# Performance work log

Hardware: AMD Instinct MI355X
Metric: run time of the kernel (lower is better)

Reference implementation:

```python
import jax, jax.numpy as jnp
import numpy as np

DIM = 4096
N_HEADS = 32
N_KV_HEADS = 8
HEAD_DIM = DIM // N_HEADS  # 128
N_REP = N_HEADS // N_KV_HEADS  # 4
MAX_BS = 16
MAX_SEQ = 4096
SEQLEN = 1
START_POS = 4095
ROPE_THETA = 500000.0


def setup_inputs() -> dict:
    key = jax.random.key(0)
    ks = jax.random.split(key, 8)
    w_scale = 0.02  # keep logits in a sane range
    x = jax.random.normal(ks[0], (MAX_BS, SEQLEN, DIM), dtype=jnp.float32)
    wq = jax.random.normal(ks[1], (DIM, N_HEADS * HEAD_DIM), dtype=jnp.float32) * w_scale
    wk = jax.random.normal(ks[2], (DIM, N_KV_HEADS * HEAD_DIM), dtype=jnp.float32) * w_scale
    wv = jax.random.normal(ks[3], (DIM, N_KV_HEADS * HEAD_DIM), dtype=jnp.float32) * w_scale
    wo = jax.random.normal(ks[4], (N_HEADS * HEAD_DIM, DIM), dtype=jnp.float32) * w_scale
    cache_k = jax.random.normal(ks[5], (MAX_BS, MAX_SEQ, N_KV_HEADS, HEAD_DIM), dtype=jnp.float32)
    cache_v = jax.random.normal(ks[6], (MAX_BS, MAX_SEQ, N_KV_HEADS, HEAD_DIM), dtype=jnp.float32)
    # true rotary frequencies for positions [START_POS, START_POS+SEQLEN)
    inv_freq = 1.0 / (ROPE_THETA ** (np.arange(0, HEAD_DIM, 2, dtype=np.float32) / HEAD_DIM))  # [hd/2]
    t = np.arange(START_POS, START_POS + SEQLEN, dtype=np.float32)[:, None]  # [s,1]
    angles = t * inv_freq[None, :]  # [s, hd/2]
    freqs_cos = jnp.asarray(np.cos(angles), dtype=jnp.float32)
    freqs_sin = jnp.asarray(np.sin(angles), dtype=jnp.float32)
    return {"x": x, "wq": wq, "wk": wk, "wv": wv, "wo": wo,
            "cache_k": cache_k, "cache_v": cache_v,
            "freqs_cos": freqs_cos, "freqs_sin": freqs_sin,
            "start_pos": START_POS}


def _rope(t, cos, sin):
    # t: [b, s, h, hd]; cos/sin: [s, hd/2] -> broadcast [1, s, 1, hd/2]
    b, s, h, hd = t.shape
    tp = t.reshape(b, s, h, hd // 2, 2)
    e, o = tp[..., 0], tp[..., 1]
    c = cos[None, :, None, :]
    sn = sin[None, :, None, :]
    re = e * c - o * sn
    im = e * sn + o * c
    return jnp.stack([re, im], axis=-1).reshape(b, s, h, hd)


def reference(x, wq, wk, wv, wo, cache_k, cache_v, freqs_cos, freqs_sin, start_pos):
    bsz, seqlen, _ = x.shape
    xq = (x @ wq).reshape(bsz, seqlen, N_HEADS, HEAD_DIM)
    xk = (x @ wk).reshape(bsz, seqlen, N_KV_HEADS, HEAD_DIM)
    xv = (x @ wv).reshape(bsz, seqlen, N_KV_HEADS, HEAD_DIM)
    xq = _rope(xq, freqs_cos, freqs_sin)
    xk = _rope(xk, freqs_cos, freqs_sin)
    # KV-cache append
    cache_k = jax.lax.dynamic_update_slice(cache_k, xk, (0, start_pos, 0, 0))
    cache_v = jax.lax.dynamic_update_slice(cache_v, xv, (0, start_pos, 0, 0))
    kv_len = start_pos + seqlen  # static Python int
    keys = cache_k[:, :kv_len]    # [b, t, g, hd]
    values = cache_v[:, :kv_len]  # [b, t, g, hd]
    # GQA via broadcasting (math-equivalent to repeat_kv)
    q = xq.reshape(bsz, seqlen, N_KV_HEADS, N_REP, HEAD_DIM)
    scale = 1.0 / jnp.sqrt(jnp.float32(HEAD_DIM))
    scores = jnp.einsum('bsgrh,btgh->bgrst', q, keys) * scale  # [b,g,r,s,t]
    probs = jax.nn.softmax(scores.astype(jnp.float32), axis=-1).astype(xq.dtype)
    out = jnp.einsum('bgrst,btgh->bsgrh', probs, values)  # [b,s,g,r,hd]
    out = out.reshape(bsz, seqlen, N_HEADS * HEAD_DIM)
    return out @ wo
```

## Files before the change

### kernel.cpp

```cpp
#include <hip/hip_runtime.h>
#include <math.h>

#define DIM    4096
#define NH     32
#define NKV    8
#define HD     128
#define BS     16
#define KVLEN  4096
#define LASTPOS 4095
#define QKV_COLS 6144
#define NKC    64

typedef float f32x4 __attribute__((ext_vector_type(4)));

#define WS_QKV   0
#define WS_ATTN  98304
#define WS_PART  163840
#define WS_PQ    2326528
#define WS_PW    8617984

__global__ __launch_bounds__(256) void qkv_projA(
    const float* __restrict__ x, const float* __restrict__ wq,
    const float* __restrict__ wk, const float* __restrict__ wv,
    float* __restrict__ pq) {
  __shared__ float xs[16 * 64];
  const int tid = threadIdx.x;
  const int col = (blockIdx.x * 256 + tid) * 2;
  const int kc = blockIdx.y;
  const int k0 = kc * 64;

  for (int i = tid; i < 1024; i += 256) {
    int b = i >> 6, k = i & 63;
    xs[i] = x[b * DIM + k0 + k];
  }
  __syncthreads();

  const float* w;
  int wstride, wcol;
  if (col < 4096)      { w = wq; wstride = 4096; wcol = col; }
  else if (col < 5120) { w = wk; wstride = 1024; wcol = col - 4096; }
  else                 { w = wv; wstride = 1024; wcol = col - 5120; }
  const float* wp = w + (size_t)k0 * wstride + wcol;

  float acc0[16], acc1[16];
#pragma unroll
  for (int b = 0; b < 16; ++b) { acc0[b] = 0.f; acc1[b] = 0.f; }

#pragma unroll 2
  for (int k = 0; k < 64; k += 4) {
    float2 w0 = *(const float2*)(wp + (size_t)(k + 0) * wstride);
    float2 w1 = *(const float2*)(wp + (size_t)(k + 1) * wstride);
    float2 w2 = *(const float2*)(wp + (size_t)(k + 2) * wstride);
    float2 w3 = *(const float2*)(wp + (size_t)(k + 3) * wstride);
#pragma unroll
    for (int b = 0; b < 16; ++b) {
      float4 xb = *(const float4*)(&xs[b * 64 + k]);
      acc0[b] += xb.x * w0.x + xb.y * w1.x + xb.z * w2.x + xb.w * w3.x;
      acc1[b] += xb.x * w0.y + xb.y * w1.y + xb.z * w2.y + xb.w * w3.y;
    }
  }
#pragma unroll
  for (int b = 0; b < 16; ++b) {
    *(float2*)(&pq[((size_t)kc * 16 + b) * QKV_COLS + col]) = make_float2(acc0[b], acc1[b]);
  }
}

__global__ __launch_bounds__(256) void qkv_projB(
    const float* __restrict__ pq, float* __restrict__ qkv,
    const float* __restrict__ fc, const float* __restrict__ fs) {
  int t = blockIdx.x * 256 + threadIdx.x;
  int b = t / 3072, pr = t % 3072;
  int col = 2 * pr;
  float e = 0.f, o = 0.f;
#pragma unroll 8
  for (int kc = 0; kc < NKC; ++kc) {
    float2 v = *(const float2*)(&pq[((size_t)kc * 16 + b) * QKV_COLS + col]);
    e += v.x; o += v.y;
  }
  float re = e, im = o;
  if (col < 5120) {
    int i = (col & 127) >> 1;
    float c = fc[i], s = fs[i];
    float scale = (col < 4096) ? 0.08838834764831845f : 1.0f;
    re = (e * c - o * s) * scale;
    im = (e * s + o * c) * scale;
  }
  *(float2*)(&qkv[b * QKV_COLS + col]) = make_float2(re, im);
}

__global__ __launch_bounds__(256, 4) void attn_partial(
    const float* __restrict__ cache_k, const float* __restrict__ cache_v,
    const float* __restrict__ qkv, float* __restrict__ part) {
  __shared__ float red[4][4][130];
  const int tid = threadIdx.x;
  const int w = tid >> 6, lane = tid & 63;
  const int p = lane >> 4, ql = lane & 15;
  const int chunk = blockIdx.x & 31;
  const int bg = blockIdx.x >> 5;
  const int b = bg >> 3, g = bg & 7;
  const int t0w = chunk * 128 + w * 32;

  const float* qbase = qkv + b * QKV_COLS + g * 512;
  f32x4 qA[4], qB[4];
#pragma unroll
  for (int h = 0; h < 4; ++h) {
    qA[h] = *(const f32x4*)(qbase + h * 128 + ql * 4);
    qB[h] = *(const f32x4*)(qbase + h * 128 + 64 + ql * 4);
  }

  const float* kbase = cache_k + ((size_t)b * 4096 * 8 + g) * 128;
  const float* xk    = qkv + b * QKV_COLS + 4096 + g * 128;

  float sv8[8];
#pragma unroll
  for (int it = 0; it < 8; ++it) {
    int t = t0w + it * 4 + p;
    const float* krow = (t == LASTPOS) ? xk : (kbase + (size_t)t * 1024);
    f32x4 k0 = *(const f32x4*)(krow + ql * 4);
    f32x4 k1 = *(const f32x4*)(krow + 64 + ql * 4);
    float s[4];
#pragma unroll
    for (int h = 0; h < 4; ++h) {
      s[h] = k0[0]*qA[h][0] + k0[1]*qA[h][1] + k0[2]*qA[h][2] + k0[3]*qA[h][3]
           + k1[0]*qB[h][0] + k1[1]*qB[h][1] + k1[2]*qB[h][2] + k1[3]*qB[h][3];
    }
#pragma unroll
    for (int off = 1; off < 16; off <<= 1) {
#pragma unroll
      for (int h = 0; h < 4; ++h) s[h] += __shfl_xor(s[h], off);
    }
    int hsel = ql & 3;
    float v = s[0];
    if (hsel == 1) v = s[1];
    if (hsel == 2) v = s[2];
    if (hsel == 3) v = s[3];
    sv8[it] = v;
  }

  float m = -1e30f;
#pragma unroll
  for (int it = 0; it < 8; ++it) m = fmaxf(m, sv8[it]);
  m = fmaxf(m, __shfl_xor(m, 16));
  m = fmaxf(m, __shfl_xor(m, 32));
  float l = 0.f;
#pragma unroll
  for (int it = 0; it < 8; ++it) { sv8[it] = __expf(sv8[it] - m); l += sv8[it]; }
  l += __shfl_xor(l, 16);
  l += __shfl_xor(l, 32);

  const float* vbase = cache_v + ((size_t)b * 4096 * 8 + g) * 128;
  const float* xv    = qkv + b * QKV_COLS + 5120 + g * 128;
  const int h2 = lane >> 5;
  const int dq = lane & 31;
  f32x4 acc[4];
#pragma unroll
  for (int h = 0; h < 4; ++h) acc[h] = (f32x4)(0.f);

#pragma unroll
  for (int jj = 0; jj < 16; ++jj) {
    int lr = 2 * jj + h2;
    int t = t0w + lr;
    const float* vrow = (t == LASTPOS) ? xv : (vbase + (size_t)t * 1024);
    f32x4 vv = *(const f32x4*)(vrow + dq * 4);
    float sreg = sv8[jj >> 1];
    int srcb = (lr & 3) << 4;
    float p0 = __shfl(sreg, srcb + 0);
    float p1 = __shfl(sreg, srcb + 1);
    float p2 = __shfl(sreg, srcb + 2);
    float p3 = __shfl(sreg, srcb + 3);
    acc[0] += p0 * vv;
    acc[1] += p1 * vv;
    acc[2] += p2 * vv;
    acc[3] += p3 * vv;
  }
#pragma unroll
  for (int h = 0; h < 4; ++h) {
    acc[h][0] += __shfl_xor(acc[h][0], 32);
    acc[h][1] += __shfl_xor(acc[h][1], 32);
    acc[h][2] += __shfl_xor(acc[h][2], 32);
    acc[h][3] += __shfl_xor(acc[h][3], 32);
  }
  if (lane < 32) {
#pragma unroll
    for (int h = 0; h < 4; ++h)
      *(f32x4*)(&red[w][h][dq * 4]) = acc[h];
  }
  if (lane < 4) { red[w][lane][128] = m; red[w][lane][129] = l; }
  __syncthreads();

  for (int item = tid; item < 512; item += 256) {
    int h = item >> 7, d = item & 127;
    float M = -1e30f;
#pragma unroll
    for (int w2 = 0; w2 < 4; ++w2) M = fmaxf(M, red[w2][h][128]);
    float num = 0.f, den = 0.f;
#pragma unroll
    for (int w2 = 0; w2 < 4; ++w2) {
      float wgt = __expf(red[w2][h][128] - M);
      num += wgt * red[w2][h][d];
      den += wgt * red[w2][h][129];
    }
    size_t pi = ((size_t)blockIdx.x * 4 + h) * 132;
    part[pi + d] = num;
    if (d == 0) { part[pi + 128] = M; part[pi + 129] = den; }
  }
}

__global__ __launch_bounds__(256) void attn_combine(
    const float* __restrict__ part, float* __restrict__ attn_out) {
  int t = blockIdx.x * 256 + threadIdx.x;
  int d = t & 127, h = (t >> 7) & 3, bg = t >> 9;
  int b = bg >> 3, g = bg & 7;
  float M = -1e30f;
  float ms[32];
#pragma unroll
  for (int c = 0; c < 32; ++c) {
    ms[c] = part[((size_t)(bg * 32 + c) * 4 + h) * 132 + 128];
    M = fmaxf(M, ms[c]);
  }
  float num = 0.f, den = 0.f;
#pragma unroll 4
  for (int c = 0; c < 32; ++c) {
    const float* pr = part + ((size_t)(bg * 32 + c) * 4 + h) * 132;
    float wgt = __expf(ms[c] - M);
    num += wgt * pr[d];
    den += wgt * pr[129];
  }
  attn_out[b * DIM + (g * 4 + h) * 128 + d] = num / den;
}

__global__ __launch_bounds__(256) void out_projA(
    const float* __restrict__ attn, const float* __restrict__ wo,
    float* __restrict__ pw) {
  __shared__ float xs[16 * 64];
  const int tid = threadIdx.x;
  const int col = (blockIdx.x * 256 + tid) * 2;
  const int kc = blockIdx.y;
  const int k0 = kc * 64;

  for (int i = tid; i < 1024; i += 256) {
    int b = i >> 6, k = i & 63;
    xs[i] = attn[b * DIM + k0 + k];
  }
  __syncthreads();

  const float* wp = wo + (size_t)k0 * 4096 + col;
  float acc0[16], acc1[16];
#pragma unroll
  for (int b = 0; b < 16; ++b) { acc0[b] = 0.f; acc1[b] = 0.f; }

#pragma unroll 2
  for (int k = 0; k < 64; k += 4) {
    float2 w0 = *(const float2*)(wp + (size_t)(k + 0) * 4096);
    float2 w1 = *(const float2*)(wp + (size_t)(k + 1) * 4096);
    float2 w2 = *(const float2*)(wp + (size_t)(k + 2) * 4096);
    float2 w3 = *(const float2*)(wp + (size_t)(k + 3) * 4096);
#pragma unroll
    for (int b = 0; b < 16; ++b) {
      float4 xb = *(const float4*)(&xs[b * 64 + k]);
      acc0[b] += xb.x * w0.x + xb.y * w1.x + xb.z * w2.x + xb.w * w3.x;
      acc1[b] += xb.x * w0.y + xb.y * w1.y + xb.z * w2.y + xb.w * w3.y;
    }
  }
#pragma unroll
  for (int b = 0; b < 16; ++b) {
    *(float2*)(&pw[((size_t)kc * 16 + b) * DIM + col]) = make_float2(acc0[b], acc1[b]);
  }
}

__global__ __launch_bounds__(256) void out_projB(
    const float* __restrict__ pw, float* __restrict__ out) {
  int t = blockIdx.x * 256 + threadIdx.x;
  int b = t >> 12, col = t & 4095;
  float sum = 0.f;
#pragma unroll 8
  for (int kc = 0; kc < NKC; ++kc)
    sum += pw[((size_t)kc * 16 + b) * DIM + col];
  out[b * DIM + col] = sum;
}

extern "C" void kernel_launch(void* const* d_in, const int* in_sizes, int n_in,
                              void* d_out, int out_size, void* d_ws, size_t ws_size,
                              hipStream_t stream) {
  const float* x  = (const float*)d_in[0];
  const float* wq = (const float*)d_in[1];
  const float* wk = (const float*)d_in[2];
  const float* wv = (const float*)d_in[3];
  const float* wo = (const float*)d_in[4];
  const float* ck = (const float*)d_in[5];
  const float* cv = (const float*)d_in[6];
  const float* fc = (const float*)d_in[7];
  const float* fs = (const float*)d_in[8];

  float* ws_f  = (float*)d_ws;
  float* qkv   = ws_f + WS_QKV;
  float* attn  = ws_f + WS_ATTN;
  float* part  = ws_f + WS_PART;
  float* pq    = ws_f + WS_PQ;
  float* pw    = ws_f + WS_PW;
  float* out   = (float*)d_out;

  qkv_projA<<<dim3(12, NKC), 256, 0, stream>>>(x, wq, wk, wv, pq);
  qkv_projB<<<192, 256, 0, stream>>>(pq, qkv, fc, fs);
  attn_partial<<<4096, 256, 0, stream>>>(ck, cv, qkv, part);
  attn_combine<<<256, 256, 0, stream>>>(part, attn);
  out_projA<<<dim3(8, NKC), 256, 0, stream>>>(attn, wo, pw);
  out_projB<<<256, 256, 0, stream>>>(pw, out);
}
```

Measured before the change: 195.2 us.

## Stage KV rows in LDS with register prefetch and online softmax across chunks

The attention partial kernel now has each 512-thread block cover one batch and all 8 KV groups over a 64-token chunk. Contiguous 4 KB KV rows are loaded with fully coalesced vector loads into shared memory, and the next 8-row stage is prefetched into registers while the current one is computed. Softmax is done online across stages, and the in-block cross-wave reduction is dropped; each wave writes its own partial. The combine kernel now merges 64 chunk partials per group with a streaming rescale. This trades the previous strided per-group global loads for better coalescing, at the cost of more partials, extra barriers and heavy LDS use (64 KB) that limits occupancy.

```diff
diff --git a/kernel.cpp b/kernel.cpp
--- a/kernel.cpp
+++ b/kernel.cpp
@@ -10,14 +10,17 @@
 #define LASTPOS 4095
 #define QKV_COLS 6144
 #define NKC    64
+#define TCHUNK 64
+#define NCHK   64
+#define NSTG   8
 
 typedef float f32x4 __attribute__((ext_vector_type(4)));
 
 #define WS_QKV   0
 #define WS_ATTN  98304
 #define WS_PART  163840
-#define WS_PQ    2326528
-#define WS_PW    8617984
+#define WS_PQ    4489216
+#define WS_PW    10780672
 
 __global__ __launch_bounds__(256) void qkv_projA(
     const float* __restrict__ x, const float* __restrict__ wq,
@@ -88,19 +91,20 @@
   *(float2*)(&qkv[b * QKV_COLS + col]) = make_float2(re, im);
 }
 
-__global__ __launch_bounds__(256, 4) void attn_partial(
+__global__ __launch_bounds__(512, 4) void attn_partial(
     const float* __restrict__ cache_k, const float* __restrict__ cache_v,
     const float* __restrict__ qkv, float* __restrict__ part) {
-  __shared__ float red[4][4][130];
+  __shared__ float ks[8192];
+  __shared__ float vs[8192];
   const int tid = threadIdx.x;
   const int w = tid >> 6, lane = tid & 63;
   const int p = lane >> 4, ql = lane & 15;
-  const int chunk = blockIdx.x & 31;
-  const int bg = blockIdx.x >> 5;
-  const int b = bg >> 3, g = bg & 7;
-  const int t0w = chunk * 128 + w * 32;
-
-  const float* qbase = qkv + b * QKV_COLS + g * 512;
+  const int hsel = ql & 3;
+  const int chunk = blockIdx.x & (NCHK - 1);
+  const int b = blockIdx.x >> 6;
+  const int t0 = chunk * TCHUNK;
+
+  const float* qbase = qkv + b * QKV_COLS + w * 512;
   f32x4 qA[4], qB[4];
 #pragma unroll
   for (int h = 0; h < 4; ++h) {
@@ -108,71 +112,115 @@
     qB[h] = *(const f32x4*)(qbase + h * 128 + 64 + ql * 4);
   }
 
-  const float* kbase = cache_k + ((size_t)b * 4096 * 8 + g) * 128;
-  const float* xk    = qkv + b * QKV_COLS + 4096 + g * 128;
-
-  float sv8[8];
-#pragma unroll
-  for (int it = 0; it < 8; ++it) {
-    int t = t0w + it * 4 + p;
-    const float* krow = (t == LASTPOS) ? xk : (kbase + (size_t)t * 1024);
-    f32x4 k0 = *(const f32x4*)(krow + ql * 4);
-    f32x4 k1 = *(const f32x4*)(krow + 64 + ql * 4);
-    float s[4];
-#pragma unroll
-    for (int h = 0; h < 4; ++h) {
-      s[h] = k0[0]*qA[h][0] + k0[1]*qA[h][1] + k0[2]*qA[h][2] + k0[3]*qA[h][3]
-           + k1[0]*qB[h][0] + k1[1]*qB[h][1] + k1[2]*qB[h][2] + k1[3]*qB[h][3];
-    }
-#pragma unroll
-    for (int off = 1; off < 16; off <<= 1) {
-#pragma unroll
-      for (int h = 0; h < 4; ++h) s[h] += __shfl_xor(s[h], off);
-    }
-    int hsel = ql & 3;
-    float v = s[0];
-    if (hsel == 1) v = s[1];
-    if (hsel == 2) v = s[2];
-    if (hsel == 3) v = s[3];
-    sv8[it] = v;
-  }
-
-  float m = -1e30f;
-#pragma unroll
-  for (int it = 0; it < 8; ++it) m = fmaxf(m, sv8[it]);
-  m = fmaxf(m, __shfl_xor(m, 16));
-  m = fmaxf(m, __shfl_xor(m, 32));
-  float l = 0.f;
-#pragma unroll
-  for (int it = 0; it < 8; ++it) { sv8[it] = __expf(sv8[it] - m); l += sv8[it]; }
-  l += __shfl_xor(l, 16);
-  l += __shfl_xor(l, 32);
-
-  const float* vbase = cache_v + ((size_t)b * 4096 * 8 + g) * 128;
-  const float* xv    = qkv + b * QKV_COLS + 5120 + g * 128;
-  const int h2 = lane >> 5;
-  const int dq = lane & 31;
+  const float* kroot = cache_k + (size_t)b * 4096 * 1024;
+  const float* vroot = cache_v + (size_t)b * 4096 * 1024;
+  const float* xk = qkv + b * QKV_COLS + 4096;
+  const float* xv = qkv + b * QKV_COLS + 5120;
+
+  float m = -1e30f, l = 0.f;
   f32x4 acc[4];
 #pragma unroll
   for (int h = 0; h < 4; ++h) acc[h] = (f32x4)(0.f);
 
-#pragma unroll
-  for (int jj = 0; jj < 16; ++jj) {
-    int lr = 2 * jj + h2;
-    int t = t0w + lr;
-    const float* vrow = (t == LASTPOS) ? xv : (vbase + (size_t)t * 1024);
-    f32x4 vv = *(const f32x4*)(vrow + dq * 4);
-    float sreg = sv8[jj >> 1];
-    int srcb = (lr & 3) << 4;
-    float p0 = __shfl(sreg, srcb + 0);
-    float p1 = __shfl(sreg, srcb + 1);
-    float p2 = __shfl(sreg, srcb + 2);
-    float p3 = __shfl(sreg, srcb + 3);
-    acc[0] += p0 * vv;
-    acc[1] += p1 * vv;
-    acc[2] += p2 * vv;
-    acc[3] += p3 * vv;
-  }
+  f32x4 kreg[4], vreg[4];
+
+#pragma unroll
+  for (int j = 0; j < 4; ++j) {
+    int flat = j * 2048 + tid * 4;
+    int row = flat >> 10, col = flat & 1023;
+    int t = t0 + row;
+    kreg[j] = *(const f32x4*)((t == LASTPOS) ? (xk + col) : (kroot + (size_t)t * 1024 + col));
+    vreg[j] = *(const f32x4*)((t == LASTPOS) ? (xv + col) : (vroot + (size_t)t * 1024 + col));
+  }
+#pragma unroll
+  for (int j = 0; j < 4; ++j) {
+    int flat = j * 2048 + tid * 4;
+    *(f32x4*)(&ks[flat]) = kreg[j];
+    *(f32x4*)(&vs[flat]) = vreg[j];
+  }
+  __syncthreads();
+
+  const int h2 = lane >> 5, dq = lane & 31;
+
+  for (int s = 0; s < NSTG; ++s) {
+    if (s + 1 < NSTG) {
+#pragma unroll
+      for (int j = 0; j < 4; ++j) {
+        int flat = j * 2048 + tid * 4;
+        int row = flat >> 10, col = flat & 1023;
+        int t = t0 + (s + 1) * 8 + row;
+        kreg[j] = *(const f32x4*)((t == LASTPOS) ? (xk + col) : (kroot + (size_t)t * 1024 + col));
+        vreg[j] = *(const f32x4*)((t == LASTPOS) ? (xv + col) : (vroot + (size_t)t * 1024 + col));
+      }
+    }
+
+    float sv[2];
+#pragma unroll
+    for (int it = 0; it < 2; ++it) {
+      int row = it * 4 + p;
+      f32x4 k0 = *(const f32x4*)(&ks[row * 1024 + w * 128 + ql * 4]);
+      f32x4 k1 = *(const f32x4*)(&ks[row * 1024 + w * 128 + 64 + ql * 4]);
+      float s4[4];
+#pragma unroll
+      for (int h = 0; h < 4; ++h) {
+        s4[h] = k0[0]*qA[h][0] + k0[1]*qA[h][1] + k0[2]*qA[h][2] + k0[3]*qA[h][3]
+              + k1[0]*qB[h][0] + k1[1]*qB[h][1] + k1[2]*qB[h][2] + k1[3]*qB[h][3];
+      }
+#pragma unroll
+      for (int off = 1; off < 16; off <<= 1) {
+#pragma unroll
+        for (int h = 0; h < 4; ++h) s4[h] += __shfl_xor(s4[h], off);
+      }
+      float v = s4[0];
+      if (hsel == 1) v = s4[1];
+      if (hsel == 2) v = s4[2];
+      if (hsel == 3) v = s4[3];
+      sv[it] = v;
+    }
+
+    float ms = fmaxf(sv[0], sv[1]);
+    ms = fmaxf(ms, __shfl_xor(ms, 16));
+    ms = fmaxf(ms, __shfl_xor(ms, 32));
+    float mnew = fmaxf(m, ms);
+    float f = __expf(m - mnew);
+    m = mnew;
+    sv[0] = __expf(sv[0] - m);
+    sv[1] = __expf(sv[1] - m);
+    float ssum = sv[0] + sv[1];
+    ssum += __shfl_xor(ssum, 16);
+    ssum += __shfl_xor(ssum, 32);
+    l = l * f + ssum;
+    float f0 = __shfl(f, 0), f1 = __shfl(f, 1), f2 = __shfl(f, 2), f3 = __shfl(f, 3);
+    acc[0] *= f0; acc[1] *= f1; acc[2] *= f2; acc[3] *= f3;
+
+#pragma unroll
+    for (int jj = 0; jj < 4; ++jj) {
+      int lr = jj * 2 + h2;
+      f32x4 vv = *(const f32x4*)(&vs[lr * 1024 + w * 128 + dq * 4]);
+      float sreg = (lr >> 2) ? sv[1] : sv[0];
+      int srcb = (lr & 3) << 4;
+      float p0 = __shfl(sreg, srcb + 0);
+      float p1 = __shfl(sreg, srcb + 1);
+      float p2 = __shfl(sreg, srcb + 2);
+      float p3 = __shfl(sreg, srcb + 3);
+      acc[0] += p0 * vv;
+      acc[1] += p1 * vv;
+      acc[2] += p2 * vv;
+      acc[3] += p3 * vv;
+    }
+
+    __syncthreads();
+    if (s + 1 < NSTG) {
+#pragma unroll
+      for (int j = 0; j < 4; ++j) {
+        int flat = j * 2048 + tid * 4;
+        *(f32x4*)(&ks[flat]) = kreg[j];
+        *(f32x4*)(&vs[flat]) = vreg[j];
+      }
+      __syncthreads();
+    }
+  }
+
 #pragma unroll
   for (int h = 0; h < 4; ++h) {
     acc[h][0] += __shfl_xor(acc[h][0], 32);
@@ -180,51 +228,32 @@
     acc[h][2] += __shfl_xor(acc[h][2], 32);
     acc[h][3] += __shfl_xor(acc[h][3], 32);
   }
+  size_t pbase = ((size_t)(blockIdx.x) * 8 + w) * 4;
   if (lane < 32) {
 #pragma unroll
     for (int h = 0; h < 4; ++h)
-      *(f32x4*)(&red[w][h][dq * 4]) = acc[h];
-  }
-  if (lane < 4) { red[w][lane][128] = m; red[w][lane][129] = l; }
-  __syncthreads();
-
-  for (int item = tid; item < 512; item += 256) {
-    int h = item >> 7, d = item & 127;
-    float M = -1e30f;
-#pragma unroll
-    for (int w2 = 0; w2 < 4; ++w2) M = fmaxf(M, red[w2][h][128]);
-    float num = 0.f, den = 0.f;
-#pragma unroll
-    for (int w2 = 0; w2 < 4; ++w2) {
-      float wgt = __expf(red[w2][h][128] - M);
-      num += wgt * red[w2][h][d];
-      den += wgt * red[w2][h][129];
-    }
-    size_t pi = ((size_t)blockIdx.x * 4 + h) * 132;
-    part[pi + d] = num;
-    if (d == 0) { part[pi + 128] = M; part[pi + 129] = den; }
+      *(f32x4*)(&part[(pbase + h) * 132 + dq * 4]) = acc[h];
+  }
+  if (lane < 4) {
+    part[(pbase + lane) * 132 + 128] = m;
+    part[(pbase + lane) * 132 + 129] = l;
   }
 }
 
 __global__ __launch_bounds__(256) void attn_combine(
     const float* __restrict__ part, float* __restrict__ attn_out) {
   int t = blockIdx.x * 256 + threadIdx.x;
-  int d = t & 127, h = (t >> 7) & 3, bg = t >> 9;
-  int b = bg >> 3, g = bg & 7;
-  float M = -1e30f;
-  float ms[32];
-#pragma unroll
-  for (int c = 0; c < 32; ++c) {
-    ms[c] = part[((size_t)(bg * 32 + c) * 4 + h) * 132 + 128];
-    M = fmaxf(M, ms[c]);
-  }
-  float num = 0.f, den = 0.f;
-#pragma unroll 4
-  for (int c = 0; c < 32; ++c) {
-    const float* pr = part + ((size_t)(bg * 32 + c) * 4 + h) * 132;
-    float wgt = __expf(ms[c] - M);
-    num += wgt * pr[d];
-    den += wgt * pr[129];
+  int d = t & 127, h = (t >> 7) & 3, g = (t >> 9) & 7, b = t >> 12;
+  float M = -1e30f, num = 0.f, den = 0.f;
+  for (int c = 0; c < NCHK; ++c) {
+    const float* pr = part + ((size_t)((b * NCHK + c) * 8 + g) * 4 + h) * 132;
+    float mc = pr[128];
+    float Mn = fmaxf(M, mc);
+    float fo = __expf(M - Mn);
+    float fcur = __expf(mc - Mn);
+    num = num * fo + fcur * pr[d];
+    den = den * fo + fcur * pr[129];
+    M = Mn;
   }
   attn_out[b * DIM + (g * 4 + h) * 128 + d] = num / den;
 }
@@ -302,7 +331,7 @@
 
   qkv_projA<<<dim3(12, NKC), 256, 0, stream>>>(x, wq, wk, wv, pq);
   qkv_projB<<<192, 256, 0, stream>>>(pq, qkv, fc, fs);
-  attn_partial<<<4096, 256, 0, stream>>>(ck, cv, qkv, part);
+  attn_partial<<<16 * NCHK, 512, 0, stream>>>(ck, cv, qkv, part);
   attn_combine<<<256, 256, 0, stream>>>(part, attn);
   out_projA<<<dim3(8, NKC), 256, 0, stream>>>(attn, wo, pw);
   out_projB<<<256, 256, 0, stream>>>(pw, out);
```

New measurement: 233.3 us. 19.5% more time.

## Split decode attention into separate score and PV kernels with larger chunks

Applied to the files above, without the earlier changes.

Splits the fused partial-attention kernel into two kernels. The first computes QK scores and a block-wide softmax max and sum over 256-token chunks, writing the probabilities to a buffer. The second reads that buffer into shared memory and does the PV accumulation. The combine step becomes an online-softmax merge over 16 chunks instead of 32, with fewer partials to reduce. In exchange it adds a kernel launch and a global round trip for the probabilities, and the K and V streams no longer overlap inside one kernel.

```diff
diff --git a/kernel.cpp b/kernel.cpp
--- a/kernel.cpp
+++ b/kernel.cpp
@@ -10,14 +10,18 @@
 #define LASTPOS 4095
 #define QKV_COLS 6144
 #define NKC    64
+#define ACHUNK 256
+#define NACH   16
 
 typedef float f32x4 __attribute__((ext_vector_type(4)));
 
 #define WS_QKV   0
 #define WS_ATTN  98304
-#define WS_PART  163840
-#define WS_PQ    2326528
-#define WS_PW    8617984
+#define WS_PBUF  163840
+#define WS_MLBUF 2260992
+#define WS_PART  2277376
+#define WS_PQ    3325952
+#define WS_PW    9617408
 
 __global__ __launch_bounds__(256) void qkv_projA(
     const float* __restrict__ x, const float* __restrict__ wq,
@@ -88,17 +92,17 @@
   *(float2*)(&qkv[b * QKV_COLS + col]) = make_float2(re, im);
 }
 
-__global__ __launch_bounds__(256, 4) void attn_partial(
-    const float* __restrict__ cache_k, const float* __restrict__ cache_v,
-    const float* __restrict__ qkv, float* __restrict__ part) {
-  __shared__ float red[4][4][130];
+__global__ __launch_bounds__(512) void attn_score(
+    const float* __restrict__ cache_k, const float* __restrict__ qkv,
+    float* __restrict__ pbuf, float* __restrict__ mlbuf) {
+  __shared__ float red[8][4][2];
   const int tid = threadIdx.x;
   const int w = tid >> 6, lane = tid & 63;
-  const int p = lane >> 4, ql = lane & 15;
-  const int chunk = blockIdx.x & 31;
-  const int bg = blockIdx.x >> 5;
-  const int b = bg >> 3, g = bg & 7;
-  const int t0w = chunk * 128 + w * 32;
+  const int p = lane >> 4, ql = lane & 15, hsel = ql & 3;
+  const int c = blockIdx.x & (NACH - 1);
+  const int g = (blockIdx.x >> 4) & 7;
+  const int b = blockIdx.x >> 7;
+  const int t0 = c * ACHUNK;
 
   const float* qbase = qkv + b * QKV_COLS + g * 512;
   f32x4 qA[4], qB[4];
@@ -111,63 +115,103 @@
   const float* kbase = cache_k + ((size_t)b * 4096 * 8 + g) * 128;
   const float* xk    = qkv + b * QKV_COLS + 4096 + g * 128;
 
-  float sv8[8];
+  float sv[8];
 #pragma unroll
   for (int it = 0; it < 8; ++it) {
-    int t = t0w + it * 4 + p;
+    int r = w * 32 + it * 4 + p;
+    int t = t0 + r;
     const float* krow = (t == LASTPOS) ? xk : (kbase + (size_t)t * 1024);
     f32x4 k0 = *(const f32x4*)(krow + ql * 4);
     f32x4 k1 = *(const f32x4*)(krow + 64 + ql * 4);
-    float s[4];
+    float s4[4];
 #pragma unroll
     for (int h = 0; h < 4; ++h) {
-      s[h] = k0[0]*qA[h][0] + k0[1]*qA[h][1] + k0[2]*qA[h][2] + k0[3]*qA[h][3]
-           + k1[0]*qB[h][0] + k1[1]*qB[h][1] + k1[2]*qB[h][2] + k1[3]*qB[h][3];
+      s4[h] = k0[0]*qA[h][0] + k0[1]*qA[h][1] + k0[2]*qA[h][2] + k0[3]*qA[h][3]
+            + k1[0]*qB[h][0] + k1[1]*qB[h][1] + k1[2]*qB[h][2] + k1[3]*qB[h][3];
     }
 #pragma unroll
     for (int off = 1; off < 16; off <<= 1) {
 #pragma unroll
-      for (int h = 0; h < 4; ++h) s[h] += __shfl_xor(s[h], off);
+      for (int h = 0; h < 4; ++h) s4[h] += __shfl_xor(s4[h], off);
     }
-    int hsel = ql & 3;
-    float v = s[0];
-    if (hsel == 1) v = s[1];
-    if (hsel == 2) v = s[2];
-    if (hsel == 3) v = s[3];
-    sv8[it] = v;
+    float v = s4[0];
+    if (hsel == 1) v = s4[1];
+    if (hsel == 2) v = s4[2];
+    if (hsel == 3) v = s4[3];
+    sv[it] = v;
   }
 
   float m = -1e30f;
 #pragma unroll
-  for (int it = 0; it < 8; ++it) m = fmaxf(m, sv8[it]);
+  for (int it = 0; it < 8; ++it) m = fmaxf(m, sv[it]);
   m = fmaxf(m, __shfl_xor(m, 16));
   m = fmaxf(m, __shfl_xor(m, 32));
+  if (lane < 4) red[w][lane][0] = m;
+  __syncthreads();
+
+  float M = -1e30f;
+#pragma unroll
+  for (int w2 = 0; w2 < 8; ++w2) M = fmaxf(M, red[w2][hsel][0]);
+
   float l = 0.f;
 #pragma unroll
-  for (int it = 0; it < 8; ++it) { sv8[it] = __expf(sv8[it] - m); l += sv8[it]; }
+  for (int it = 0; it < 8; ++it) { sv[it] = __expf(sv[it] - M); l += sv[it]; }
   l += __shfl_xor(l, 16);
   l += __shfl_xor(l, 32);
+  if (lane < 4) red[w][lane][1] = l;
+  __syncthreads();
+
+  if (tid < 4) {
+    float L = 0.f;
+#pragma unroll
+    for (int w2 = 0; w2 < 8; ++w2) L += red[w2][tid][1];
+    size_t mi = ((size_t)blockIdx.x * 4 + tid) * 2;
+    mlbuf[mi + 0] = M;
+    mlbuf[mi + 1] = L;
+  }
+
+  if (ql < 4) {
+    float* pp = pbuf + ((size_t)blockIdx.x * 4 + hsel) * 256;
+#pragma unroll
+    for (int it = 0; it < 8; ++it)
+      pp[w * 32 + it * 4 + p] = sv[it];
+  }
+}
+
+__global__ __launch_bounds__(512) void attn_pv(
+    const float* __restrict__ cache_v, const float* __restrict__ qkv,
+    const float* __restrict__ pbuf, float* __restrict__ part) {
+  __shared__ float ss[4 * 256];
+  __shared__ float pacc[8][4][128];
+  const int tid = threadIdx.x;
+  const int w = tid >> 6, lane = tid & 63;
+  const int c = blockIdx.x & (NACH - 1);
+  const int g = (blockIdx.x >> 4) & 7;
+  const int b = blockIdx.x >> 7;
+  const int t0 = c * ACHUNK;
+
+  const float* pp = pbuf + (size_t)blockIdx.x * 1024;
+  for (int i = tid; i < 1024; i += 512) ss[i] = pp[i];
+  __syncthreads();
 
   const float* vbase = cache_v + ((size_t)b * 4096 * 8 + g) * 128;
   const float* xv    = qkv + b * QKV_COLS + 5120 + g * 128;
-  const int h2 = lane >> 5;
-  const int dq = lane & 31;
+  const int h2 = lane >> 5, dq = lane & 31;
+
   f32x4 acc[4];
 #pragma unroll
   for (int h = 0; h < 4; ++h) acc[h] = (f32x4)(0.f);
 
 #pragma unroll
   for (int jj = 0; jj < 16; ++jj) {
-    int lr = 2 * jj + h2;
-    int t = t0w + lr;
+    int lr = w * 32 + 2 * jj + h2;
+    int t = t0 + lr;
     const float* vrow = (t == LASTPOS) ? xv : (vbase + (size_t)t * 1024);
     f32x4 vv = *(const f32x4*)(vrow + dq * 4);
-    float sreg = sv8[jj >> 1];
-    int srcb = (lr & 3) << 4;
-    float p0 = __shfl(sreg, srcb + 0);
-    float p1 = __shfl(sreg, srcb + 1);
-    float p2 = __shfl(sreg, srcb + 2);
-    float p3 = __shfl(sreg, srcb + 3);
+    float p0 = ss[0 * 256 + lr];
+    float p1 = ss[1 * 256 + lr];
+    float p2 = ss[2 * 256 + lr];
+    float p3 = ss[3 * 256 + lr];
     acc[0] += p0 * vv;
     acc[1] += p1 * vv;
     acc[2] += p2 * vv;
@@ -183,48 +227,36 @@
   if (lane < 32) {
 #pragma unroll
     for (int h = 0; h < 4; ++h)
-      *(f32x4*)(&red[w][h][dq * 4]) = acc[h];
-  }
-  if (lane < 4) { red[w][lane][128] = m; red[w][lane][129] = l; }
-  __syncthreads();
-
-  for (int item = tid; item < 512; item += 256) {
-    int h = item >> 7, d = item & 127;
-    float M = -1e30f;
-#pragma unroll
-    for (int w2 = 0; w2 < 4; ++w2) M = fmaxf(M, red[w2][h][128]);
-    float num = 0.f, den = 0.f;
-#pragma unroll
-    for (int w2 = 0; w2 < 4; ++w2) {
-      float wgt = __expf(red[w2][h][128] - M);
-      num += wgt * red[w2][h][d];
-      den += wgt * red[w2][h][129];
-    }
-    size_t pi = ((size_t)blockIdx.x * 4 + h) * 132;
-    part[pi + d] = num;
-    if (d == 0) { part[pi + 128] = M; part[pi + 129] = den; }
+      *(f32x4*)(&pacc[w][h][dq * 4]) = acc[h];
+  }
+  __syncthreads();
+
+  {
+    int h = tid >> 7, d = tid & 127;
+    float sum = 0.f;
+#pragma unroll
+    for (int w2 = 0; w2 < 8; ++w2) sum += pacc[w2][h][d];
+    part[((size_t)blockIdx.x * 4 + h) * 128 + d] = sum;
   }
 }
 
 __global__ __launch_bounds__(256) void attn_combine(
-    const float* __restrict__ part, float* __restrict__ attn_out) {
+    const float* __restrict__ part, const float* __restrict__ mlbuf,
+    float* __restrict__ attn_out) {
   int t = blockIdx.x * 256 + threadIdx.x;
-  int d = t & 127, h = (t >> 7) & 3, bg = t >> 9;
-  int b = bg >> 3, g = bg & 7;
-  float M = -1e30f;
-  float ms[32];
-#pragma unroll
-  for (int c = 0; c < 32; ++c) {
-    ms[c] = part[((size_t)(bg * 32 + c) * 4 + h) * 132 + 128];
-    M = fmaxf(M, ms[c]);
-  }
-  float num = 0.f, den = 0.f;
+  int d = t & 127, h = (t >> 7) & 3, g = (t >> 9) & 7, b = t >> 12;
+  float M = -1e30f, num = 0.f, den = 0.f;
 #pragma unroll 4
-  for (int c = 0; c < 32; ++c) {
-    const float* pr = part + ((size_t)(bg * 32 + c) * 4 + h) * 132;
-    float wgt = __expf(ms[c] - M);
-    num += wgt * pr[d];
-    den += wgt * pr[129];
+  for (int c = 0; c < NACH; ++c) {
+    size_t blk = ((size_t)b << 7) | (g << 4) | c;
+    float mc = mlbuf[(blk * 4 + h) * 2 + 0];
+    float lc = mlbuf[(blk * 4 + h) * 2 + 1];
+    float Mn = fmaxf(M, mc);
+    float fo = __expf(M - Mn);
+    float fcur = __expf(mc - Mn);
+    num = num * fo + fcur * part[(blk * 4 + h) * 128 + d];
+    den = den * fo + fcur * lc;
+    M = Mn;
   }
   attn_out[b * DIM + (g * 4 + h) * 128 + d] = num / den;
 }
@@ -295,6 +327,8 @@
   float* ws_f  = (float*)d_ws;
   float* qkv   = ws_f + WS_QKV;
   float* attn  = ws_f + WS_ATTN;
+  float* pbuf  = ws_f + WS_PBUF;
+  float* mlbuf = ws_f + WS_MLBUF;
   float* part  = ws_f + WS_PART;
   float* pq    = ws_f + WS_PQ;
   float* pw    = ws_f + WS_PW;
@@ -302,8 +336,9 @@
 
   qkv_projA<<<dim3(12, NKC), 256, 0, stream>>>(x, wq, wk, wv, pq);
   qkv_projB<<<192, 256, 0, stream>>>(pq, qkv, fc, fs);
-  attn_partial<<<4096, 256, 0, stream>>>(ck, cv, qkv, part);
-  attn_combine<<<256, 256, 0, stream>>>(part, attn);
+  attn_score<<<16 * 8 * NACH, 512, 0, stream>>>(ck, qkv, pbuf, mlbuf);
+  attn_pv<<<16 * 8 * NACH, 512, 0, stream>>>(cv, qkv, pbuf, part);
+  attn_combine<<<256, 256, 0, stream>>>(part, mlbuf, attn);
   out_projA<<<dim3(8, NKC), 256, 0, stream>>>(attn, wo, pw);
   out_projB<<<256, 256, 0, stream>>>(pw, out);
 }
```

Result: slower. 200.3 us (+2.6%).
